# Kernel tuning notes

Hardware: AMD Instinct MI355X
Metric: run time of the kernel (lower is better)

## Reference

```python
import jax, jax.numpy as jnp
import numpy as np

VOCAB = 32000
EMBED = 128


def setup_inputs() -> dict:
    key = jax.random.key(0)
    k1, k2, k3 = jax.random.split(key, 3)
    e = jax.random.randint(k1, (4, 2048), 0, VOCAB)            # token ids
    W = jax.random.normal(k2, (EMBED, VOCAB), dtype=jnp.float32) * 0.02  # nn.Linear weight [out,in]
    b = jax.random.normal(k3, (EMBED,), dtype=jnp.float32) * 0.02        # nn.Linear bias
    return {"e": e, "W": W, "b": b}


def reference(e, W, b):
    # Original: one_hot(e, VOCAB) @ W.T + b. Mathematically identical to
    # gathering column e of W (a standard embedding lookup) plus bias.
    # out[b, s, :] = W[:, e[b, s]] + b
    out = jnp.take(W.T, e, axis=0) + b  # [4, 2048, EMBED]
    return out
```

## Files before the change

### kernel.cpp

```cpp
#include <hip/hip_runtime.h>
#include <hip/hip_bf16.h>

#define VOCAB 32000
#define EMBED 128
#define NTOK  (4 * 2048)
#define TV    64
#define PITCH 129

__global__ __launch_bounds__(256) void embed_tile(const int* __restrict__ e,
                                                  const float* __restrict__ W,
                                                  const float* __restrict__ bias,
                                                  float* __restrict__ out) {
    __shared__ float ldsT[TV * PITCH];

    const int tid   = threadIdx.x;
    const int v0    = blockIdx.x * TV;
    const int lane  = tid & 63;
    const int wid   = tid >> 6;
    const int wbase = wid * (NTOK / 4);

    int4 ebuf[8];
    #pragma unroll
    for (int s = 0; s < 8; ++s)
        ebuf[s] = *reinterpret_cast<const int4*>(&e[wbase + (s << 8) + (lane << 2)]);

    {
        const int c4 = (tid & 15) << 2;
        const int dr = tid >> 4;
        #pragma unroll
        for (int it = 0; it < 8; ++it) {
            const int d = dr + (it << 4);
            float4 w = *reinterpret_cast<const float4*>(&W[d * VOCAB + v0 + c4]);
            const float bd = bias[d];
            ldsT[(c4 + 0) * PITCH + d] = w.x + bd;
            ldsT[(c4 + 1) * PITCH + d] = w.y + bd;
            ldsT[(c4 + 2) * PITCH + d] = w.z + bd;
            ldsT[(c4 + 3) * PITCH + d] = w.w + bd;
        }
    }
    __syncthreads();

    const int l2 = lane << 1;
    #pragma unroll
    for (int s = 0; s < 8; ++s) {
        const int tok[4] = {ebuf[s].x, ebuf[s].y, ebuf[s].z, ebuf[s].w};
        #pragma unroll
        for (int j = 0; j < 4; ++j) {
            const unsigned c = (unsigned)(tok[j] - v0);
            unsigned long long m = __ballot(c < TV);
            while (m) {
                const int src = __builtin_ctzll(m);
                m &= m - 1;
                const int cc = __shfl((int)c, src, 64);
                const int tt = wbase + (s << 8) + (src << 2) + j;
                const float2 v = *reinterpret_cast<const float2*>(&ldsT[cc * PITCH + l2]);
                *reinterpret_cast<float2*>(&out[tt * EMBED + l2]) = v;
            }
        }
    }
}

extern "C" void kernel_launch(void* const* d_in, const int* in_sizes, int n_in,
                              void* d_out, int out_size, void* d_ws, size_t ws_size,
                              hipStream_t stream) {
    const int*   e    = (const int*)d_in[0];
    const float* W    = (const float*)d_in[1];
    const float* bias = (const float*)d_in[2];
    float*       out  = (float*)d_out;

    const int grid = VOCAB / TV;
    embed_tile<<<grid, 256, 0, stream>>>(e, W, bias, out);
}
```

Measured before the change: 9.955 us.

## Load W tile directly to LDS via global_load_lds, move bias add to gather

Replaces the register-staged transposed LDS fill with direct global-to-LDS async loads (global_load_lds, 16 bytes per lane) in the natural d-major layout, and applies the bias at gather time from registers. Block size doubles to 512 threads, so each wave scans 1024 tokens instead of 2048, halving the per-wave ballot loop. The gather now reads two strided LDS words per hit (stride TV=64 floats), which may cause bank conflicts compared with the earlier contiguous float2 read.

```diff
diff --git a/kernel.cpp b/kernel.cpp
--- a/kernel.cpp
+++ b/kernel.cpp
@@ -5,44 +5,42 @@
 #define EMBED 128
 #define NTOK  (4 * 2048)
 #define TV    64
-#define PITCH 129
+#define BLK   512
 
-__global__ __launch_bounds__(256) void embed_tile(const int* __restrict__ e,
+__global__ __launch_bounds__(BLK) void embed_tile(const int* __restrict__ e,
                                                   const float* __restrict__ W,
                                                   const float* __restrict__ bias,
                                                   float* __restrict__ out) {
-    __shared__ float ldsT[TV * PITCH];
+    __shared__ float lds[EMBED * TV];
 
-    const int tid   = threadIdx.x;
-    const int v0    = blockIdx.x * TV;
-    const int lane  = tid & 63;
-    const int wid   = tid >> 6;
-    const int wbase = wid * (NTOK / 4);
+    const int tid  = threadIdx.x;
+    const int lane = tid & 63;
+    const int wid  = tid >> 6;
+    const int v0   = blockIdx.x * TV;
 
-    int4 ebuf[8];
+    const int wbase = wid << 10;
+    int4 ebuf[4];
     #pragma unroll
-    for (int s = 0; s < 8; ++s)
+    for (int s = 0; s < 4; ++s)
         ebuf[s] = *reinterpret_cast<const int4*>(&e[wbase + (s << 8) + (lane << 2)]);
 
-    {
-        const int c4 = (tid & 15) << 2;
-        const int dr = tid >> 4;
-        #pragma unroll
-        for (int it = 0; it < 8; ++it) {
-            const int d = dr + (it << 4);
-            float4 w = *reinterpret_cast<const float4*>(&W[d * VOCAB + v0 + c4]);
-            const float bd = bias[d];
-            ldsT[(c4 + 0) * PITCH + d] = w.x + bd;
-            ldsT[(c4 + 1) * PITCH + d] = w.y + bd;
-            ldsT[(c4 + 2) * PITCH + d] = w.z + bd;
-            ldsT[(c4 + 3) * PITCH + d] = w.w + bd;
-        }
+    const float2 bl = *reinterpret_cast<const float2*>(&bias[lane << 1]);
+
+    #pragma unroll
+    for (int i = 0; i < 4; ++i) {
+        const int k = (wid << 2) + i;
+        const int d = (k << 2) + (lane >> 4);
+        const int c = (lane & 15) << 2;
+        __builtin_amdgcn_global_load_lds(
+            (const __attribute__((address_space(1))) void*)(&W[d * VOCAB + v0 + c]),
+            (__attribute__((address_space(3))) void*)(&lds[k << 8]),
+            16, 0, 0);
     }
     __syncthreads();
 
     const int l2 = lane << 1;
     #pragma unroll
-    for (int s = 0; s < 8; ++s) {
+    for (int s = 0; s < 4; ++s) {
         const int tok[4] = {ebuf[s].x, ebuf[s].y, ebuf[s].z, ebuf[s].w};
         #pragma unroll
         for (int j = 0; j < 4; ++j) {
@@ -53,7 +51,9 @@
                 m &= m - 1;
                 const int cc = __shfl((int)c, src, 64);
                 const int tt = wbase + (s << 8) + (src << 2) + j;
-                const float2 v = *reinterpret_cast<const float2*>(&ldsT[cc * PITCH + l2]);
+                float2 v;
+                v.x = lds[(l2 + 0) * TV + cc] + bl.x;
+                v.y = lds[(l2 + 1) * TV + cc] + bl.y;
                 *reinterpret_cast<float2*>(&out[tt * EMBED + l2]) = v;
             }
         }
@@ -69,5 +69,5 @@
     float*       out  = (float*)d_out;
 
     const int grid = VOCAB / TV;
-    embed_tile<<<grid, 256, 0, stream>>>(e, W, bias, out);
+    embed_tile<<<grid, BLK, 0, stream>>>(e, W, bias, out);
 }
```

New measurement: 10.21 us. +2.6%, slower.
